# Kernel optimization log

Measured on AMD Instinct MI355X. Metric: run time of the kernel, lower is better.

## Reference

```python
import jax, jax.numpy as jnp
from jax import lax
import numpy as np

H = 20  # hardcoded n_hidden in the module


def _lstm_layer(xs, W_ih, W_hh, b):
    """xs: [T, B, F] -> hs: [T, B, H]. PyTorch gate order i,f,g,o."""
    B = xs.shape[1]
    h0 = jnp.zeros((B, H), xs.dtype)
    c0 = jnp.zeros((B, H), xs.dtype)

    def step(carry, x_t):
        h, c = carry
        g = x_t @ W_ih.T + h @ W_hh.T + b  # [B, 4H]
        i, f, gg, o = jnp.split(g, 4, axis=-1)
        c = jax.nn.sigmoid(f) * c + jax.nn.sigmoid(i) * jnp.tanh(gg)
        h = jax.nn.sigmoid(o) * jnp.tanh(c)
        return (h, c), h

    _, hs = lax.scan(step, (h0, c0), xs)
    return hs


def setup_inputs() -> dict:
    key = jax.random.key(0)
    ks = jax.random.split(key, 9)
    B, T, F, C = 1024, 512, 64, 10
    s_in = 1.0 / np.sqrt(H)
    return {
        "x": jax.random.normal(ks[0], (B, T, F), jnp.float32),
        "W_ih0": jax.random.uniform(ks[1], (4 * H, F), jnp.float32, -s_in, s_in),
        "W_hh0": jax.random.uniform(ks[2], (4 * H, H), jnp.float32, -s_in, s_in),
        "b0": jax.random.uniform(ks[3], (4 * H,), jnp.float32, -s_in, s_in),
        "W_ih1": jax.random.uniform(ks[4], (4 * H, H), jnp.float32, -s_in, s_in),
        "W_hh1": jax.random.uniform(ks[5], (4 * H, H), jnp.float32, -s_in, s_in),
        "b1": jax.random.uniform(ks[6], (4 * H,), jnp.float32, -s_in, s_in),
        "W_fc": jax.random.uniform(ks[7], (C, H * T), jnp.float32, -0.01, 0.01),
        "b_fc": jax.random.uniform(ks[8], (C,), jnp.float32, -0.01, 0.01),
    }


def reference(x, W_ih0, W_hh0, b0, W_ih1, W_hh1, b1, W_fc, b_fc):
    B = x.shape[0]
    xs = jnp.transpose(x, (1, 0, 2))          # [T, B, F]
    hs = _lstm_layer(xs, W_ih0, W_hh0, b0)    # [T, B, H]
    hs = _lstm_layer(hs, W_ih1, W_hh1, b1)    # [T, B, H]
    flat = jnp.transpose(hs, (1, 0, 2)).reshape(B, -1)  # [B, T*H]
    return flat @ W_fc.T + b_fc
```

## Files before the change

kernel.cpp:

```cpp
#include <hip/hip_runtime.h>

#define T_STEPS 512
#define F_IN    64
#define HID     20
#define NCLS    10
#define BATCH   1024

typedef __attribute__((ext_vector_type(8))) short bf16x8;
typedef __attribute__((ext_vector_type(4))) float f32x4;
typedef __attribute__((ext_vector_type(2))) float f32x2;

__device__ __forceinline__ float rcpf(float x) { return __builtin_amdgcn_rcpf(x); }
__device__ __forceinline__ float bperm(int idxBytes, float v) {
    return __int_as_float(__builtin_amdgcn_ds_bpermute(idxBytes, __float_as_int(v)));
}
__device__ __forceinline__ unsigned short bf16h(float v) {
    unsigned u = __float_as_uint(v);
    return (unsigned short)((u + 0x7fffu + ((u >> 16) & 1u)) >> 16);
}
__device__ __forceinline__ float bf16f(unsigned short h) {
    return __uint_as_float(((unsigned)h) << 16);
}
__device__ __forceinline__ f32x2 pkfma(f32x2 a, f32x2 b, f32x2 c) {
    f32x2 d;
    asm("v_pk_fma_f32 %0, %1, %2, %3" : "=v"(d) : "v"(a), "v"(b), "v"(c));
    return d;
}

extern "C" __global__ __launch_bounds__(256, 2)
void zgemm_mfma(const float* __restrict__ x, const float* __restrict__ W,
                const float* __restrict__ b0, float* __restrict__ Z)
{
    __shared__ unsigned short xlds[4][2][32][72];

    const int tid = threadIdx.x;
    const int w   = tid >> 6;
    const int l   = tid & 63;
    const int ar  = l & 15;
    const int aq  = l >> 4;
    const size_t R0 = ((size_t)blockIdx.x * 4 + w) * 32;

    const float* xw = x + R0 * F_IN;
    #pragma unroll
    for (int i = 0; i < 8; ++i) {
        const int idx = (i << 6) + l;
        const int row = idx >> 4;
        const int c4  = idx & 15;
        const float4 v = *(const float4*)(xw + (row << 6) + (c4 << 2));
        const unsigned short h0 = bf16h(v.x), h1 = bf16h(v.y),
                             h2 = bf16h(v.z), h3 = bf16h(v.w);
        const unsigned short g0 = bf16h(v.x - bf16f(h0)), g1 = bf16h(v.y - bf16f(h1)),
                             g2 = bf16h(v.z - bf16f(h2)), g3 = bf16h(v.w - bf16f(h3));
        *(uint2*)&xlds[w][0][row][c4 << 2] =
            make_uint2((unsigned)h0 | ((unsigned)h1 << 16), (unsigned)h2 | ((unsigned)h3 << 16));
        *(uint2*)&xlds[w][1][row][c4 << 2] =
            make_uint2((unsigned)g0 | ((unsigned)g1 << 16), (unsigned)g2 | ((unsigned)g3 << 16));
    }
    __syncthreads();

    bf16x8 af[2][2][2];
    #pragma unroll
    for (int m = 0; m < 2; ++m)
        #pragma unroll
        for (int s = 0; s < 2; ++s) {
            af[m][s][0] = *(const bf16x8*)&xlds[w][0][m * 16 + ar][aq * 8 + s * 32];
            af[m][s][1] = *(const bf16x8*)&xlds[w][1][m * 16 + ar][aq * 8 + s * 32];
        }

    bf16x8 bfr[5][2][2];
    #pragma unroll
    for (int n = 0; n < 5; ++n)
        #pragma unroll
        for (int s = 0; s < 2; ++s) {
            const float* wp = W + (size_t)(n * 16 + ar) * F_IN + aq * 8 + s * 32;
            const float4 u = *(const float4*)wp;
            const float4 v = *(const float4*)(wp + 4);
            bf16x8 hf, gf;
            hf[0] = (short)bf16h(u.x); gf[0] = (short)bf16h(u.x - bf16f(bf16h(u.x)));
            hf[1] = (short)bf16h(u.y); gf[1] = (short)bf16h(u.y - bf16f(bf16h(u.y)));
            hf[2] = (short)bf16h(u.z); gf[2] = (short)bf16h(u.z - bf16f(bf16h(u.z)));
            hf[3] = (short)bf16h(u.w); gf[3] = (short)bf16h(u.w - bf16f(bf16h(u.w)));
            hf[4] = (short)bf16h(v.x); gf[4] = (short)bf16h(v.x - bf16f(bf16h(v.x)));
            hf[5] = (short)bf16h(v.y); gf[5] = (short)bf16h(v.y - bf16f(bf16h(v.y)));
            hf[6] = (short)bf16h(v.z); gf[6] = (short)bf16h(v.z - bf16f(bf16h(v.z)));
            hf[7] = (short)bf16h(v.w); gf[7] = (short)bf16h(v.w - bf16f(bf16h(v.w)));
            bfr[n][s][0] = hf;
            bfr[n][s][1] = gf;
        }

    #pragma unroll
    for (int m = 0; m < 2; ++m)
        #pragma unroll
        for (int n = 0; n < 5; ++n) {
            const float bb = b0[n * 16 + ar];
            f32x4 acc = {bb, bb, bb, bb};
            #pragma unroll
            for (int s = 0; s < 2; ++s) {
                acc = __builtin_amdgcn_mfma_f32_16x16x32_bf16(af[m][s][0], bfr[n][s][0], acc, 0, 0, 0);
                acc = __builtin_amdgcn_mfma_f32_16x16x32_bf16(af[m][s][0], bfr[n][s][1], acc, 0, 0, 0);
                acc = __builtin_amdgcn_mfma_f32_16x16x32_bf16(af[m][s][1], bfr[n][s][0], acc, 0, 0, 0);
            }
            float* zp = Z + (R0 + m * 16 + aq * 4) * 80 + n * 16 + ar;
            zp[0]   = acc[0];
            zp[80]  = acc[1];
            zp[160] = acc[2];
            zp[240] = acc[3];
        }
}

extern "C" __global__ __launch_bounds__(128, 2)
void lstm_rec(const float* __restrict__ Z0,
              const float* __restrict__ W_hh0,
              const float* __restrict__ W_ih1, const float* __restrict__ W_hh1,
              const float* __restrict__ b1,
              const float* __restrict__ W_fc, const float* __restrict__ b_fc,
              float* __restrict__ out)
{
    __shared__ float4 ringH0v[4][6];
    __shared__ float4 ringH1v[8][6];
    float* ringH0 = (float*)ringH0v;
    float* ringH1 = (float*)ringH1v;

    const int tid = threadIdx.x;
    const int l   = tid & 63;
    const int wid = tid >> 6;
    const int b   = blockIdx.x;
    const int g2  = 64 + (l & 15);
    const bool isG = (l >= 40 && l < 60);

    const float mnegP = isG ? -2.885390082f : -1.442695041f;
    const float sclP  = isG ? 2.0f : 1.0f;
    const float biaP  = isG ? -1.0f : 0.0f;

    const int idxF  = ((l + 20) & 63) << 2;
    const int idxG  = ((l + 40) & 63) << 2;
    const int idxO  = ((l + 60) & 63) << 2;
    const int idxOB = ((l -  4) & 63) << 2;

    for (int i = tid; i < 96; i += 128)  ringH0[i] = 0.f;
    for (int i = tid; i < 192; i += 128) ringH1[i] = 0.f;

    f32x2 wh0p2[10], wh0s2[10];
    float c0 = 0.f;
    float zpc = 0.f, zsc = 0.f, zpn = 0.f, zsn = 0.f;
    unsigned zP = 0, zS = 0;
    const char* Zb = (const char*)Z0;
    #define ZLD(o) (*(const float*)(Zb + (o)))
    f32x2 facc2 = {0.f, 0.f};
    float4 wfc = make_float4(0.f, 0.f, 0.f, 0.f);
    unsigned wfOff = 0;
    int c4off = 0;
    const char* Wfb = (const char*)W_fc;

    f32x2 wi1p2[10], wi1s2[10], wh1p2[10], wh1s2[10];
    float b1p = 0.f, b1s = 0.f;
    float c1 = 0.f;

    if (wid == 0) {
        const f32x2* p;
        p = (const f32x2*)(W_hh0 + l  * HID);
        #pragma unroll
        for (int k = 0; k < 10; ++k) wh0p2[k] = p[k];
        p = (const f32x2*)(W_hh0 + g2 * HID);
        #pragma unroll
        for (int k = 0; k < 10; ++k) wh0s2[k] = p[k];

        zP = (unsigned)((b * (T_STEPS * 80) + l) * 4);
        zS = (unsigned)((b * (T_STEPS * 80) + 64 + (l & 15)) * 4);
        zpc = ZLD(zP);       zsc = ZLD(zS);
        zpn = ZLD(zP + 320); zsn = ZLD(zS + 320);
        zP += 640; zS += 640;

        const int cls = (l < 50) ? (l / 5) : 0;
        const int c4  = (l < 50) ? (l % 5) : 0;
        c4off = c4 * 16;
        wfOff = (unsigned)((cls * (T_STEPS * HID) + c4 * 4) * 4);
    } else {
        const f32x2* p;
        p = (const f32x2*)(W_ih1 + l  * HID);
        #pragma unroll
        for (int k = 0; k < 10; ++k) wi1p2[k] = p[k];
        p = (const f32x2*)(W_ih1 + g2 * HID);
        #pragma unroll
        for (int k = 0; k < 10; ++k) wi1s2[k] = p[k];
        p = (const f32x2*)(W_hh1 + l  * HID);
        #pragma unroll
        for (int k = 0; k < 10; ++k) wh1p2[k] = p[k];
        p = (const f32x2*)(W_hh1 + g2 * HID);
        #pragma unroll
        for (int k = 0; k < 10; ++k) wh1s2[k] = p[k];
        b1p = b1[l];
        b1s = b1[g2];
    }
    __syncthreads();

    #pragma unroll 8
    for (int t = 0; t < T_STEPS + 4; ++t) {
        if (wid == 0) {
            const int sigma = t - 4;
            float4 wfn = make_float4(0.f, 0.f, 0.f, 0.f);
            if (t >= 3 && t < T_STEPS + 3) {
                wfn = *(const float4*)(Wfb + wfOff);
                wfOff += HID * 4;
            }
            if (t < T_STEPS) {
                const float zp = zpc, zs = zsc;
                zpc = zpn; zsc = zsn;
                if (t + 2 < T_STEPS) {
                    zpn = ZLD(zP); zsn = ZLD(zS);
                    zP += 320; zS += 320;
                }
                f32x2 h2[10];
                {
                    const f32x4* hp = (const f32x4*)(ringH0 + ((t + 3) & 3) * 24);
                    #pragma unroll
                    for (int k = 0; k < 5; ++k) {
                        const f32x4 v = hp[k];
                        h2[2 * k]     = __builtin_shufflevector(v, v, 0, 1);
                        h2[2 * k + 1] = __builtin_shufflevector(v, v, 2, 3);
                    }
                }
                f32x2 aP = {zp, 0.f}, aP1 = {0.f, 0.f};
                f32x2 aS = {zs, 0.f}, aS1 = {0.f, 0.f};
                #pragma unroll
                for (int j = 0; j < 5; ++j) {
                    aP  = pkfma(h2[j],     wh0p2[j],     aP);
                    aP1 = pkfma(h2[5 + j], wh0p2[5 + j], aP1);
                    aS  = pkfma(h2[j],     wh0s2[j],     aS);
                    aS1 = pkfma(h2[5 + j], wh0s2[5 + j], aS1);
                }
                const float a_p = (aP.x + aP1.x) + (aP.y + aP1.y);
                const float a_s = (aS.x + aS1.x) + (aS.y + aS1.y);
                const float actP = fmaf(rcpf(1.f + exp2f(a_p * mnegP)), sclP, biaP);
                const float actS = rcpf(1.f + exp2f(a_s * -1.442695041f));
                const float fv = bperm(idxF, actP), gv = bperm(idxG, actP);
                const float oA = bperm(idxO, actP), oB = bperm(idxOB, actS);
                const float ov = (l < 4) ? oA : oB;
                c0 = fmaf(fv, c0, actP * gv);
                const float h0v = ov * fmaf(rcpf(1.f + exp2f(c0 * -2.885390082f)), 2.f, -1.f);
                if (l < HID) ringH0[(t & 3) * 24 + l] = h0v;
            }
            if (sigma >= 0) {
                const float4 h1q = *(const float4*)((const char*)ringH1 +
                                                    ((sigma & 7) * 96) + c4off);
                facc2 = pkfma((f32x2){h1q.x, h1q.y}, (f32x2){wfc.x, wfc.y}, facc2);
                facc2 = pkfma((f32x2){h1q.z, h1q.w}, (f32x2){wfc.z, wfc.w}, facc2);
            }
            wfc = wfn;
        } else {
            const int tau = t - 2;
            if (tau >= 0 && tau < T_STEPS) {
                f32x2 h02[10], h12[10];
                {
                    const f32x4* hp = (const f32x4*)(ringH0 + (tau & 3) * 24);
                    const f32x4* hq = (const f32x4*)(ringH1 + ((tau + 7) & 7) * 24);
                    #pragma unroll
                    for (int k = 0; k < 5; ++k) {
                        const f32x4 v = hp[k];
                        const f32x4 u = hq[k];
                        h02[2 * k]     = __builtin_shufflevector(v, v, 0, 1);
                        h02[2 * k + 1] = __builtin_shufflevector(v, v, 2, 3);
                        h12[2 * k]     = __builtin_shufflevector(u, u, 0, 1);
                        h12[2 * k + 1] = __builtin_shufflevector(u, u, 2, 3);
                    }
                }
                f32x2 bP = {b1p, 0.f}, bP1 = {0.f, 0.f};
                f32x2 bS = {b1s, 0.f}, bS1 = {0.f, 0.f};
                #pragma unroll
                for (int j = 0; j < 5; ++j) {
                    bP  = pkfma(h12[j],     wh1p2[j],     bP);
                    bP1 = pkfma(h12[5 + j], wh1p2[5 + j], bP1);
                    bS  = pkfma(h12[j],     wh1s2[j],     bS);
                    bS1 = pkfma(h12[5 + j], wh1s2[5 + j], bS1);
                }
                #pragma unroll
                for (int j = 0; j < 5; ++j) {
                    bP  = pkfma(h02[j],     wi1p2[j],     bP);
                    bP1 = pkfma(h02[5 + j], wi1p2[5 + j], bP1);
                    bS  = pkfma(h02[j],     wi1s2[j],     bS);
                    bS1 = pkfma(h02[5 + j], wi1s2[5 + j], bS1);
                }
                const float b_p = (bP.x + bP1.x) + (bP.y + bP1.y);
                const float b_s = (bS.x + bS1.x) + (bS.y + bS1.y);
                const float actQ = fmaf(rcpf(1.f + exp2f(b_p * mnegP)), sclP, biaP);
                const float actT = rcpf(1.f + exp2f(b_s * -1.442695041f));
                const float fv = bperm(idxF, actQ), gv = bperm(idxG, actQ);
                const float oA = bperm(idxO, actQ), oB = bperm(idxOB, actT);
                const float ov = (l < 4) ? oA : oB;
                c1 = fmaf(fv, c1, actQ * gv);
                const float h1v = ov * fmaf(rcpf(1.f + exp2f(c1 * -2.885390082f)), 2.f, -1.f);
                if (l < HID) ringH1[(tau & 7) * 24 + l] = h1v;
            }
        }
        if (t & 1) {
            asm volatile("s_waitcnt lgkmcnt(0)" ::: "memory");
            __builtin_amdgcn_s_barrier();
            asm volatile("" ::: "memory");
        }
    }

    if (wid == 0) {
        const float f = facc2.x + facc2.y;
        float r = f;
        r += __shfl(f, l + 1);
        r += __shfl(f, l + 2);
        r += __shfl(f, l + 3);
        r += __shfl(f, l + 4);
        if (l < 50 && (l % 5) == 0)
            out[(size_t)b * NCLS + (l / 5)] = r + b_fc[l / 5];
    }
}

extern "C" void kernel_launch(void* const* d_in, const int* in_sizes, int n_in,
                              void* d_out, int out_size, void* d_ws, size_t ws_size,
                              hipStream_t stream) {
    const float* x     = (const float*)d_in[0];
    const float* W_ih0 = (const float*)d_in[1];
    const float* W_hh0 = (const float*)d_in[2];
    const float* b0    = (const float*)d_in[3];
    const float* W_ih1 = (const float*)d_in[4];
    const float* W_hh1 = (const float*)d_in[5];
    const float* b1    = (const float*)d_in[6];
    const float* W_fc  = (const float*)d_in[7];
    const float* b_fc  = (const float*)d_in[8];
    float* out = (float*)d_out;

    float* Z0 = (float*)d_ws;

    zgemm_mfma<<<dim3(4096), dim3(256), 0, stream>>>(x, W_ih0, b0, Z0);
    lstm_rec<<<dim3(BATCH), dim3(128), 0, stream>>>(Z0, W_hh0, W_ih1, W_hh1,
                                                    b1, W_fc, b_fc, out);
}
```

Measured before the change: 318.6 us.

## Interleave LSTM gate rows per quad and gather gates with DPP instead of bpermute

Gate rows are remapped so that each quad of lanes holds the i,f,g,o pre-activations for one hidden unit, and the gates are gathered with DPP quad broadcasts instead of LDS bpermute. Hidden units 16-19 are handled by a second duplicated set of accumulators. The h0 ring buffer is doubled, the layer-1 and FC skews are lengthened, and the block barrier now fires every 4 steps instead of every 2. The aim is to take the LDS-latency permute ops off the recurrent critical path and to synchronise less often. The cost is extra activation math for the second set and deeper ring buffers.

New measurement: 341.5 us. 1.07x slower.

```diff
diff --git a/kernel.cpp b/kernel.cpp
--- a/kernel.cpp
+++ b/kernel.cpp
@@ -11,9 +11,6 @@
 typedef __attribute__((ext_vector_type(2))) float f32x2;
 
 __device__ __forceinline__ float rcpf(float x) { return __builtin_amdgcn_rcpf(x); }
-__device__ __forceinline__ float bperm(int idxBytes, float v) {
-    return __int_as_float(__builtin_amdgcn_ds_bpermute(idxBytes, __float_as_int(v)));
-}
 __device__ __forceinline__ unsigned short bf16h(float v) {
     unsigned u = __float_as_uint(v);
     return (unsigned short)((u + 0x7fffu + ((u >> 16) & 1u)) >> 16);
@@ -25,6 +22,10 @@
     f32x2 d;
     asm("v_pk_fma_f32 %0, %1, %2, %3" : "=v"(d) : "v"(a), "v"(b), "v"(c));
     return d;
+}
+template<int CTRL>
+__device__ __forceinline__ float qb(float v) {
+    return __int_as_float(__builtin_amdgcn_mov_dpp(__float_as_int(v), CTRL, 0xF, 0xF, true));
 }
 
 extern "C" __global__ __launch_bounds__(256, 2)
@@ -116,7 +117,7 @@
               const float* __restrict__ W_fc, const float* __restrict__ b_fc,
               float* __restrict__ out)
 {
-    __shared__ float4 ringH0v[4][6];
+    __shared__ float4 ringH0v[8][6];
     __shared__ float4 ringH1v[8][6];
     float* ringH0 = (float*)ringH0v;
     float* ringH1 = (float*)ringH1v;
@@ -125,23 +126,20 @@
     const int l   = tid & 63;
     const int wid = tid >> 6;
     const int b   = blockIdx.x;
-    const int g2  = 64 + (l & 15);
-    const bool isG = (l >= 40 && l < 60);
+    const int p   = l & 3;
+    const int q   = l >> 2;
+    const int rp  = p * HID + q;
+    const int rsc = p * HID + 16 + (q & 3);
+    const bool isG = (p == 2);
 
     const float mnegP = isG ? -2.885390082f : -1.442695041f;
     const float sclP  = isG ? 2.0f : 1.0f;
     const float biaP  = isG ? -1.0f : 0.0f;
 
-    const int idxF  = ((l + 20) & 63) << 2;
-    const int idxG  = ((l + 40) & 63) << 2;
-    const int idxO  = ((l + 60) & 63) << 2;
-    const int idxOB = ((l -  4) & 63) << 2;
-
-    for (int i = tid; i < 96; i += 128)  ringH0[i] = 0.f;
-    for (int i = tid; i < 192; i += 128) ringH1[i] = 0.f;
+    for (int i = tid; i < 192; i += 128) { ringH0[i] = 0.f; ringH1[i] = 0.f; }
 
     f32x2 wh0p2[10], wh0s2[10];
-    float c0 = 0.f;
+    float c0p = 0.f, c0s = 0.f;
     float zpc = 0.f, zsc = 0.f, zpn = 0.f, zsn = 0.f;
     unsigned zP = 0, zS = 0;
     const char* Zb = (const char*)Z0;
@@ -154,19 +152,19 @@
 
     f32x2 wi1p2[10], wi1s2[10], wh1p2[10], wh1s2[10];
     float b1p = 0.f, b1s = 0.f;
-    float c1 = 0.f;
+    float c1p = 0.f, c1s = 0.f;
 
     if (wid == 0) {
-        const f32x2* p;
-        p = (const f32x2*)(W_hh0 + l  * HID);
-        #pragma unroll
-        for (int k = 0; k < 10; ++k) wh0p2[k] = p[k];
-        p = (const f32x2*)(W_hh0 + g2 * HID);
-        #pragma unroll
-        for (int k = 0; k < 10; ++k) wh0s2[k] = p[k];
-
-        zP = (unsigned)((b * (T_STEPS * 80) + l) * 4);
-        zS = (unsigned)((b * (T_STEPS * 80) + 64 + (l & 15)) * 4);
+        const f32x2* wp;
+        wp = (const f32x2*)(W_hh0 + rp * HID);
+        #pragma unroll
+        for (int k = 0; k < 10; ++k) wh0p2[k] = wp[k];
+        wp = (const f32x2*)(W_hh0 + rsc * HID);
+        #pragma unroll
+        for (int k = 0; k < 10; ++k) wh0s2[k] = wp[k];
+
+        zP = (unsigned)((b * (T_STEPS * 80) + rp) * 4);
+        zS = (unsigned)((b * (T_STEPS * 80) + rsc) * 4);
         zpc = ZLD(zP);       zsc = ZLD(zS);
         zpn = ZLD(zP + 320); zsn = ZLD(zS + 320);
         zP += 640; zS += 640;
@@ -176,30 +174,30 @@
         c4off = c4 * 16;
         wfOff = (unsigned)((cls * (T_STEPS * HID) + c4 * 4) * 4);
     } else {
-        const f32x2* p;
-        p = (const f32x2*)(W_ih1 + l  * HID);
-        #pragma unroll
-        for (int k = 0; k < 10; ++k) wi1p2[k] = p[k];
-        p = (const f32x2*)(W_ih1 + g2 * HID);
-        #pragma unroll
-        for (int k = 0; k < 10; ++k) wi1s2[k] = p[k];
-        p = (const f32x2*)(W_hh1 + l  * HID);
-        #pragma unroll
-        for (int k = 0; k < 10; ++k) wh1p2[k] = p[k];
-        p = (const f32x2*)(W_hh1 + g2 * HID);
-        #pragma unroll
-        for (int k = 0; k < 10; ++k) wh1s2[k] = p[k];
-        b1p = b1[l];
-        b1s = b1[g2];
+        const f32x2* wp;
+        wp = (const f32x2*)(W_ih1 + rp * HID);
+        #pragma unroll
+        for (int k = 0; k < 10; ++k) wi1p2[k] = wp[k];
+        wp = (const f32x2*)(W_ih1 + rsc * HID);
+        #pragma unroll
+        for (int k = 0; k < 10; ++k) wi1s2[k] = wp[k];
+        wp = (const f32x2*)(W_hh1 + rp * HID);
+        #pragma unroll
+        for (int k = 0; k < 10; ++k) wh1p2[k] = wp[k];
+        wp = (const f32x2*)(W_hh1 + rsc * HID);
+        #pragma unroll
+        for (int k = 0; k < 10; ++k) wh1s2[k] = wp[k];
+        b1p = b1[rp];
+        b1s = b1[rsc];
     }
     __syncthreads();
 
     #pragma unroll 8
-    for (int t = 0; t < T_STEPS + 4; ++t) {
+    for (int t = 0; t < T_STEPS + 8; ++t) {
         if (wid == 0) {
-            const int sigma = t - 4;
+            const int sigma = t - 8;
             float4 wfn = make_float4(0.f, 0.f, 0.f, 0.f);
-            if (t >= 3 && t < T_STEPS + 3) {
+            if (t >= 7 && t < T_STEPS + 7) {
                 wfn = *(const float4*)(Wfb + wfOff);
                 wfOff += HID * 4;
             }
@@ -212,7 +210,7 @@
                 }
                 f32x2 h2[10];
                 {
-                    const f32x4* hp = (const f32x4*)(ringH0 + ((t + 3) & 3) * 24);
+                    const f32x4* hp = (const f32x4*)(ringH0 + ((t + 7) & 7) * 24);
                     #pragma unroll
                     for (int k = 0; k < 5; ++k) {
                         const f32x4 v = hp[k];
@@ -232,13 +230,19 @@
                 const float a_p = (aP.x + aP1.x) + (aP.y + aP1.y);
                 const float a_s = (aS.x + aS1.x) + (aS.y + aS1.y);
                 const float actP = fmaf(rcpf(1.f + exp2f(a_p * mnegP)), sclP, biaP);
-                const float actS = rcpf(1.f + exp2f(a_s * -1.442695041f));
-                const float fv = bperm(idxF, actP), gv = bperm(idxG, actP);
-                const float oA = bperm(idxO, actP), oB = bperm(idxOB, actS);
-                const float ov = (l < 4) ? oA : oB;
-                c0 = fmaf(fv, c0, actP * gv);
-                const float h0v = ov * fmaf(rcpf(1.f + exp2f(c0 * -2.885390082f)), 2.f, -1.f);
-                if (l < HID) ringH0[(t & 3) * 24 + l] = h0v;
+                const float actS = fmaf(rcpf(1.f + exp2f(a_s * mnegP)), sclP, biaP);
+                const float iP = qb<0x00>(actP), fP = qb<0x55>(actP),
+                            gP = qb<0xAA>(actP), oP = qb<0xFF>(actP);
+                c0p = fmaf(fP, c0p, iP * gP);
+                const float hP = oP * fmaf(rcpf(1.f + exp2f(c0p * -2.885390082f)), 2.f, -1.f);
+                const float iS = qb<0x00>(actS), fS = qb<0x55>(actS),
+                            gS = qb<0xAA>(actS), oS = qb<0xFF>(actS);
+                c0s = fmaf(fS, c0s, iS * gS);
+                const float hS = oS * fmaf(rcpf(1.f + exp2f(c0s * -2.885390082f)), 2.f, -1.f);
+                if (p == 0) {
+                    ringH0[(t & 7) * 24 + q] = hP;
+                    if (l < 16) ringH0[(t & 7) * 24 + 16 + q] = hS;
+                }
             }
             if (sigma >= 0) {
                 const float4 h1q = *(const float4*)((const char*)ringH1 +
@@ -248,11 +252,11 @@
             }
             wfc = wfn;
         } else {
-            const int tau = t - 2;
+            const int tau = t - 4;
             if (tau >= 0 && tau < T_STEPS) {
                 f32x2 h02[10], h12[10];
                 {
-                    const f32x4* hp = (const f32x4*)(ringH0 + (tau & 3) * 24);
+                    const f32x4* hp = (const f32x4*)(ringH0 + (tau & 7) * 24);
                     const f32x4* hq = (const f32x4*)(ringH1 + ((tau + 7) & 7) * 24);
                     #pragma unroll
                     for (int k = 0; k < 5; ++k) {
@@ -283,16 +287,22 @@
                 const float b_p = (bP.x + bP1.x) + (bP.y + bP1.y);
                 const float b_s = (bS.x + bS1.x) + (bS.y + bS1.y);
                 const float actQ = fmaf(rcpf(1.f + exp2f(b_p * mnegP)), sclP, biaP);
-                const float actT = rcpf(1.f + exp2f(b_s * -1.442695041f));
-                const float fv = bperm(idxF, actQ), gv = bperm(idxG, actQ);
-                const float oA = bperm(idxO, actQ), oB = bperm(idxOB, actT);
-                const float ov = (l < 4) ? oA : oB;
-                c1 = fmaf(fv, c1, actQ * gv);
-                const float h1v = ov * fmaf(rcpf(1.f + exp2f(c1 * -2.885390082f)), 2.f, -1.f);
-                if (l < HID) ringH1[(tau & 7) * 24 + l] = h1v;
-            }
-        }
-        if (t & 1) {
+                const float actT = fmaf(rcpf(1.f + exp2f(b_s * mnegP)), sclP, biaP);
+                const float iP = qb<0x00>(actQ), fP = qb<0x55>(actQ),
+                            gP = qb<0xAA>(actQ), oP = qb<0xFF>(actQ);
+                c1p = fmaf(fP, c1p, iP * gP);
+                const float hP = oP * fmaf(rcpf(1.f + exp2f(c1p * -2.885390082f)), 2.f, -1.f);
+                const float iS = qb<0x00>(actT), fS = qb<0x55>(actT),
+                            gS = qb<0xAA>(actT), oS = qb<0xFF>(actT);
+                c1s = fmaf(fS, c1s, iS * gS);
+                const float hS = oS * fmaf(rcpf(1.f + exp2f(c1s * -2.885390082f)), 2.f, -1.f);
+                if (p == 0) {
+                    ringH1[(tau & 7) * 24 + q] = hP;
+                    if (l < 16) ringH1[(tau & 7) * 24 + 16 + q] = hS;
+                }
+            }
+        }
+        if ((t & 3) == 3) {
             asm volatile("s_waitcnt lgkmcnt(0)" ::: "memory");
             __builtin_amdgcn_s_barrier();
             asm volatile("" ::: "memory");
```

## Process two batch rows per block in LSTM recurrence with deeper pipeline

Applied to the files above, without the earlier changes.

Each recurrence block now handles two batch elements, interleaving their independent dependency chains inside each wave to expose instruction-level parallelism. Ring buffers are duplicated per element and deepened to 8 slots. The layer-1 and FC lags are lengthened accordingly, and the grid is halved. This trades thread-level parallelism (fewer resident waves) and higher register pressure for better latency hiding per wave.

After: 496.6 us. +55.9%, slower.

```diff
diff --git a/kernel.cpp b/kernel.cpp
--- a/kernel.cpp
+++ b/kernel.cpp
@@ -108,7 +108,7 @@
         }
 }
 
-extern "C" __global__ __launch_bounds__(128, 2)
+extern "C" __global__ __launch_bounds__(128, 1)
 void lstm_rec(const float* __restrict__ Z0,
               const float* __restrict__ W_hh0,
               const float* __restrict__ W_ih1, const float* __restrict__ W_hh1,
@@ -116,15 +116,15 @@
               const float* __restrict__ W_fc, const float* __restrict__ b_fc,
               float* __restrict__ out)
 {
-    __shared__ float4 ringH0v[4][6];
-    __shared__ float4 ringH1v[8][6];
+    __shared__ float4 ringH0v[2][8][6];
+    __shared__ float4 ringH1v[2][8][6];
     float* ringH0 = (float*)ringH0v;
     float* ringH1 = (float*)ringH1v;
 
     const int tid = threadIdx.x;
     const int l   = tid & 63;
     const int wid = tid >> 6;
-    const int b   = blockIdx.x;
+    const int bb  = blockIdx.x * 2;
     const int g2  = 64 + (l & 15);
     const bool isG = (l >= 40 && l < 60);
 
@@ -137,16 +137,15 @@
     const int idxO  = ((l + 60) & 63) << 2;
     const int idxOB = ((l -  4) & 63) << 2;
 
-    for (int i = tid; i < 96; i += 128)  ringH0[i] = 0.f;
-    for (int i = tid; i < 192; i += 128) ringH1[i] = 0.f;
+    for (int i = tid; i < 384; i += 128) { ringH0[i] = 0.f; ringH1[i] = 0.f; }
 
     f32x2 wh0p2[10], wh0s2[10];
-    float c0 = 0.f;
-    float zpc = 0.f, zsc = 0.f, zpn = 0.f, zsn = 0.f;
-    unsigned zP = 0, zS = 0;
+    float c0[2] = {0.f, 0.f};
+    float zpc[2], zsc[2], zpn[2], zsn[2];
+    unsigned zP[2], zS[2];
     const char* Zb = (const char*)Z0;
     #define ZLD(o) (*(const float*)(Zb + (o)))
-    f32x2 facc2 = {0.f, 0.f};
+    f32x2 facc[2] = {{0.f, 0.f}, {0.f, 0.f}};
     float4 wfc = make_float4(0.f, 0.f, 0.f, 0.f);
     unsigned wfOff = 0;
     int c4off = 0;
@@ -154,142 +153,180 @@
 
     f32x2 wi1p2[10], wi1s2[10], wh1p2[10], wh1s2[10];
     float b1p = 0.f, b1s = 0.f;
-    float c1 = 0.f;
+    float c1[2] = {0.f, 0.f};
 
     if (wid == 0) {
-        const f32x2* p;
-        p = (const f32x2*)(W_hh0 + l  * HID);
-        #pragma unroll
-        for (int k = 0; k < 10; ++k) wh0p2[k] = p[k];
-        p = (const f32x2*)(W_hh0 + g2 * HID);
-        #pragma unroll
-        for (int k = 0; k < 10; ++k) wh0s2[k] = p[k];
-
-        zP = (unsigned)((b * (T_STEPS * 80) + l) * 4);
-        zS = (unsigned)((b * (T_STEPS * 80) + 64 + (l & 15)) * 4);
-        zpc = ZLD(zP);       zsc = ZLD(zS);
-        zpn = ZLD(zP + 320); zsn = ZLD(zS + 320);
-        zP += 640; zS += 640;
+        const f32x2* wp;
+        wp = (const f32x2*)(W_hh0 + l  * HID);
+        #pragma unroll
+        for (int k = 0; k < 10; ++k) wh0p2[k] = wp[k];
+        wp = (const f32x2*)(W_hh0 + g2 * HID);
+        #pragma unroll
+        for (int k = 0; k < 10; ++k) wh0s2[k] = wp[k];
+
+        #pragma unroll
+        for (int e = 0; e < 2; ++e) {
+            zP[e] = (unsigned)(((bb + e) * (T_STEPS * 80) + l) * 4);
+            zS[e] = (unsigned)(((bb + e) * (T_STEPS * 80) + 64 + (l & 15)) * 4);
+            zpc[e] = ZLD(zP[e]);       zsc[e] = ZLD(zS[e]);
+            zpn[e] = ZLD(zP[e] + 320); zsn[e] = ZLD(zS[e] + 320);
+            zP[e] += 640; zS[e] += 640;
+        }
 
         const int cls = (l < 50) ? (l / 5) : 0;
         const int c4  = (l < 50) ? (l % 5) : 0;
         c4off = c4 * 16;
         wfOff = (unsigned)((cls * (T_STEPS * HID) + c4 * 4) * 4);
     } else {
-        const f32x2* p;
-        p = (const f32x2*)(W_ih1 + l  * HID);
-        #pragma unroll
-        for (int k = 0; k < 10; ++k) wi1p2[k] = p[k];
-        p = (const f32x2*)(W_ih1 + g2 * HID);
-        #pragma unroll
-        for (int k = 0; k < 10; ++k) wi1s2[k] = p[k];
-        p = (const f32x2*)(W_hh1 + l  * HID);
-        #pragma unroll
-        for (int k = 0; k < 10; ++k) wh1p2[k] = p[k];
-        p = (const f32x2*)(W_hh1 + g2 * HID);
-        #pragma unroll
-        for (int k = 0; k < 10; ++k) wh1s2[k] = p[k];
+        const f32x2* wp;
+        wp = (const f32x2*)(W_ih1 + l  * HID);
+        #pragma unroll
+        for (int k = 0; k < 10; ++k) wi1p2[k] = wp[k];
+        wp = (const f32x2*)(W_ih1 + g2 * HID);
+        #pragma unroll
+        for (int k = 0; k < 10; ++k) wi1s2[k] = wp[k];
+        wp = (const f32x2*)(W_hh1 + l  * HID);
+        #pragma unroll
+        for (int k = 0; k < 10; ++k) wh1p2[k] = wp[k];
+        wp = (const f32x2*)(W_hh1 + g2 * HID);
+        #pragma unroll
+        for (int k = 0; k < 10; ++k) wh1s2[k] = wp[k];
         b1p = b1[l];
         b1s = b1[g2];
     }
     __syncthreads();
 
-    #pragma unroll 8
-    for (int t = 0; t < T_STEPS + 4; ++t) {
+    #pragma unroll 4
+    for (int t = 0; t < T_STEPS + 8; ++t) {
         if (wid == 0) {
-            const int sigma = t - 4;
+            const int sigma = t - 8;
             float4 wfn = make_float4(0.f, 0.f, 0.f, 0.f);
-            if (t >= 3 && t < T_STEPS + 3) {
+            if (t >= 7 && t < T_STEPS + 7) {
                 wfn = *(const float4*)(Wfb + wfOff);
                 wfOff += HID * 4;
             }
             if (t < T_STEPS) {
-                const float zp = zpc, zs = zsc;
-                zpc = zpn; zsc = zsn;
+                float zp[2], zs[2];
+                #pragma unroll
+                for (int e = 0; e < 2; ++e) {
+                    zp[e] = zpc[e]; zs[e] = zsc[e];
+                    zpc[e] = zpn[e]; zsc[e] = zsn[e];
+                }
                 if (t + 2 < T_STEPS) {
-                    zpn = ZLD(zP); zsn = ZLD(zS);
-                    zP += 320; zS += 320;
-                }
-                f32x2 h2[10];
-                {
-                    const f32x4* hp = (const f32x4*)(ringH0 + ((t + 3) & 3) * 24);
+                    #pragma unroll
+                    for (int e = 0; e < 2; ++e) {
+                        zpn[e] = ZLD(zP[e]); zsn[e] = ZLD(zS[e]);
+                        zP[e] += 320; zS[e] += 320;
+                    }
+                }
+                f32x2 h2[2][10];
+                #pragma unroll
+                for (int e = 0; e < 2; ++e) {
+                    const f32x4* hp = (const f32x4*)(ringH0 + e * 192 + ((t + 7) & 7) * 24);
                     #pragma unroll
                     for (int k = 0; k < 5; ++k) {
                         const f32x4 v = hp[k];
-                        h2[2 * k]     = __builtin_shufflevector(v, v, 0, 1);
-                        h2[2 * k + 1] = __builtin_shufflevector(v, v, 2, 3);
-                    }
-                }
-                f32x2 aP = {zp, 0.f}, aP1 = {0.f, 0.f};
-                f32x2 aS = {zs, 0.f}, aS1 = {0.f, 0.f};
+                        h2[e][2 * k]     = __builtin_shufflevector(v, v, 0, 1);
+                        h2[e][2 * k + 1] = __builtin_shufflevector(v, v, 2, 3);
+                    }
+                }
+                f32x2 aP[2], aP1[2], aS[2], aS1[2];
+                #pragma unroll
+                for (int e = 0; e < 2; ++e) {
+                    aP[e] = (f32x2){zp[e], 0.f}; aP1[e] = (f32x2){0.f, 0.f};
+                    aS[e] = (f32x2){zs[e], 0.f}; aS1[e] = (f32x2){0.f, 0.f};
+                }
                 #pragma unroll
                 for (int j = 0; j < 5; ++j) {
-                    aP  = pkfma(h2[j],     wh0p2[j],     aP);
-                    aP1 = pkfma(h2[5 + j], wh0p2[5 + j], aP1);
-                    aS  = pkfma(h2[j],     wh0s2[j],     aS);
-                    aS1 = pkfma(h2[5 + j], wh0s2[5 + j], aS1);
-                }
-                const float a_p = (aP.x + aP1.x) + (aP.y + aP1.y);
-                const float a_s = (aS.x + aS1.x) + (aS.y + aS1.y);
-                const float actP = fmaf(rcpf(1.f + exp2f(a_p * mnegP)), sclP, biaP);
-                const float actS = rcpf(1.f + exp2f(a_s * -1.442695041f));
-                const float fv = bperm(idxF, actP), gv = bperm(idxG, actP);
-                const float oA = bperm(idxO, actP), oB = bperm(idxOB, actS);
-                const float ov = (l < 4) ? oA : oB;
-                c0 = fmaf(fv, c0, actP * gv);
-                const float h0v = ov * fmaf(rcpf(1.f + exp2f(c0 * -2.885390082f)), 2.f, -1.f);
-                if (l < HID) ringH0[(t & 3) * 24 + l] = h0v;
+                    #pragma unroll
+                    for (int e = 0; e < 2; ++e) {
+                        aP[e]  = pkfma(h2[e][j],     wh0p2[j],     aP[e]);
+                        aP1[e] = pkfma(h2[e][5 + j], wh0p2[5 + j], aP1[e]);
+                        aS[e]  = pkfma(h2[e][j],     wh0s2[j],     aS[e]);
+                        aS1[e] = pkfma(h2[e][5 + j], wh0s2[5 + j], aS1[e]);
+                    }
+                }
+                #pragma unroll
+                for (int e = 0; e < 2; ++e) {
+                    const float a_p = (aP[e].x + aP1[e].x) + (aP[e].y + aP1[e].y);
+                    const float a_s = (aS[e].x + aS1[e].x) + (aS[e].y + aS1[e].y);
+                    const float actP = fmaf(rcpf(1.f + exp2f(a_p * mnegP)), sclP, biaP);
+                    const float actS = rcpf(1.f + exp2f(a_s * -1.442695041f));
+                    const float fv = bperm(idxF, actP), gv = bperm(idxG, actP);
+                    const float oA = bperm(idxO, actP), oB = bperm(idxOB, actS);
+                    const float ov = (l < 4) ? oA : oB;
+                    c0[e] = fmaf(fv, c0[e], actP * gv);
+                    const float h0v = ov * fmaf(rcpf(1.f + exp2f(c0[e] * -2.885390082f)), 2.f, -1.f);
+                    if (l < HID) ringH0[e * 192 + (t & 7) * 24 + l] = h0v;
+                }
             }
             if (sigma >= 0) {
-                const float4 h1q = *(const float4*)((const char*)ringH1 +
-                                                    ((sigma & 7) * 96) + c4off);
-                facc2 = pkfma((f32x2){h1q.x, h1q.y}, (f32x2){wfc.x, wfc.y}, facc2);
-                facc2 = pkfma((f32x2){h1q.z, h1q.w}, (f32x2){wfc.z, wfc.w}, facc2);
+                #pragma unroll
+                for (int e = 0; e < 2; ++e) {
+                    const float4 h1q = *(const float4*)((const char*)ringH1 +
+                                                        e * 768 + ((sigma & 7) * 96) + c4off);
+                    facc[e] = pkfma((f32x2){h1q.x, h1q.y}, (f32x2){wfc.x, wfc.y}, facc[e]);
+                    facc[e] = pkfma((f32x2){h1q.z, h1q.w}, (f32x2){wfc.z, wfc.w}, facc[e]);
+                }
             }
             wfc = wfn;
         } else {
-            const int tau = t - 2;
+            const int tau = t - 4;
             if (tau >= 0 && tau < T_STEPS) {
-                f32x2 h02[10], h12[10];
-                {
-                    const f32x4* hp = (const f32x4*)(ringH0 + (tau & 3) * 24);
-                    const f32x4* hq = (const f32x4*)(ringH1 + ((tau + 7) & 7) * 24);
+                f32x2 h02[2][10], h12[2][10];
+                #pragma unroll
+                for (int e = 0; e < 2; ++e) {
+                    const f32x4* hp = (const f32x4*)(ringH0 + e * 192 + (tau & 7) * 24);
+                    const f32x4* hq = (const f32x4*)(ringH1 + e * 192 + ((tau + 7) & 7) * 24);
                     #pragma unroll
                     for (int k = 0; k < 5; ++k) {
                         const f32x4 v = hp[k];
                         const f32x4 u = hq[k];
-                        h02[2 * k]     = __builtin_shufflevector(v, v, 0, 1);
-                        h02[2 * k + 1] = __builtin_shufflevector(v, v, 2, 3);
-                        h12[2 * k]     = __builtin_shufflevector(u, u, 0, 1);
-                        h12[2 * k + 1] = __builtin_shufflevector(u, u, 2, 3);
-                    }
-                }
-                f32x2 bP = {b1p, 0.f}, bP1 = {0.f, 0.f};
-                f32x2 bS = {b1s, 0.f}, bS1 = {0.f, 0.f};
+                        h02[e][2 * k]     = __builtin_shufflevector(v, v, 0, 1);
+                        h02[e][2 * k + 1] = __builtin_shufflevector(v, v, 2, 3);
+                        h12[e][2 * k]     = __builtin_shufflevector(u, u, 0, 1);
+                        h12[e][2 * k + 1] = __builtin_shufflevector(u, u, 2, 3);
+                    }
+                }
+                f32x2 bP[2], bP1[2], bS[2], bS1[2];
+                #pragma unroll
+                for (int e = 0; e < 2; ++e) {
+                    bP[e] = (f32x2){b1p, 0.f}; bP1[e] = (f32x2){0.f, 0.f};
+                    bS[e] = (f32x2){b1s, 0.f}; bS1[e] = (f32x2){0.f, 0.f};
+                }
                 #pragma unroll
                 for (int j = 0; j < 5; ++j) {
-                    bP  = pkfma(h12[j],     wh1p2[j],     bP);
-                    bP1 = pkfma(h12[5 + j], wh1p2[5 + j], bP1);
-                    bS  = pkfma(h12[j],     wh1s2[j],     bS);
-                    bS1 = pkfma(h12[5 + j], wh1s2[5 + j], bS1);
+                    #pragma unroll
+                    for (int e = 0; e < 2; ++e) {
+                        bP[e]  = pkfma(h12[e][j],     wh1p2[j],     bP[e]);
+                        bP1[e] = pkfma(h12[e][5 + j], wh1p2[5 + j], bP1[e]);
+                        bS[e]  = pkfma(h12[e][j],     wh1s2[j],     bS[e]);
+                        bS1[e] = pkfma(h12[e][5 + j], wh1s2[5 + j], bS1[e]);
+                    }
                 }
                 #pragma unroll
                 for (int j = 0; j < 5; ++j) {
-                    bP  = pkfma(h02[j],     wi1p2[j],     bP);
-                    bP1 = pkfma(h02[5 + j], wi1p2[5 + j], bP1);
-                    bS  = pkfma(h02[j],     wi1s2[j],     bS);
-                    bS1 = pkfma(h02[5 + j], wi1s2[5 + j], bS1);
-                }
-                const float b_p = (bP.x + bP1.x) + (bP.y + bP1.y);
-                const float b_s = (bS.x + bS1.x) + (bS.y + bS1.y);
-                const float actQ = fmaf(rcpf(1.f + exp2f(b_p * mnegP)), sclP, biaP);
-                const float actT = rcpf(1.f + exp2f(b_s * -1.442695041f));
-                const float fv = bperm(idxF, actQ), gv = bperm(idxG, actQ);
-                const float oA = bperm(idxO, actQ), oB = bperm(idxOB, actT);
-                const float ov = (l < 4) ? oA : oB;
-                c1 = fmaf(fv, c1, actQ * gv);
-                const float h1v = ov * fmaf(rcpf(1.f + exp2f(c1 * -2.885390082f)), 2.f, -1.f);
-                if (l < HID) ringH1[(tau & 7) * 24 + l] = h1v;
+                    #pragma unroll
+                    for (int e = 0; e < 2; ++e) {
+                        bP[e]  = pkfma(h02[e][j],     wi1p2[j],     bP[e]);
+                        bP1[e] = pkfma(h02[e][5 + j], wi1p2[5 + j], bP1[e]);
+                        bS[e]  = pkfma(h02[e][j],     wi1s2[j],     bS[e]);
+                        bS1[e] = pkfma(h02[e][5 + j], wi1s2[5 + j], bS1[e]);
+                    }
+                }
+                #pragma unroll
+                for (int e = 0; e < 2; ++e) {
+                    const float b_p = (bP[e].x + bP1[e].x) + (bP[e].y + bP1[e].y);
+                    const float b_s = (bS[e].x + bS1[e].x) + (bS[e].y + bS1[e].y);
+                    const float actQ = fmaf(rcpf(1.f + exp2f(b_p * mnegP)), sclP, biaP);
+                    const float actT = rcpf(1.f + exp2f(b_s * -1.442695041f));
+                    const float fv = bperm(idxF, actQ), gv = bperm(idxG, actQ);
+                    const float oA = bperm(idxO, actQ), oB = bperm(idxOB, actT);
+                    const float ov = (l < 4) ? oA : oB;
+                    c1[e] = fmaf(fv, c1[e], actQ * gv);
+                    const float h1v = ov * fmaf(rcpf(1.f + exp2f(c1[e] * -2.885390082f)), 2.f, -1.f);
+                    if (l < HID) ringH1[e * 192 + (tau & 7) * 24 + l] = h1v;
+                }
             }
         }
         if (t & 1) {
@@ -300,14 +337,17 @@
     }
 
     if (wid == 0) {
-        const float f = facc2.x + facc2.y;
-        float r = f;
-        r += __shfl(f, l + 1);
-        r += __shfl(f, l + 2);
-        r += __shfl(f, l + 3);
-        r += __shfl(f, l + 4);
-        if (l < 50 && (l % 5) == 0)
-            out[(size_t)b * NCLS + (l / 5)] = r + b_fc[l / 5];
+        #pragma unroll
+        for (int e = 0; e < 2; ++e) {
+            const float f = facc[e].x + facc[e].y;
+            float r = f;
+            r += __shfl(f, l + 1);
+            r += __shfl(f, l + 2);
+            r += __shfl(f, l + 3);
+            r += __shfl(f, l + 4);
+            if (l < 50 && (l % 5) == 0)
+                out[(size_t)(bb + e) * NCLS + (l / 5)] = r + b_fc[l / 5];
+        }
     }
 }
 
@@ -328,6 +368,6 @@
     float* Z0 = (float*)d_ws;
 
     zgemm_mfma<<<dim3(4096), dim3(256), 0, stream>>>(x, W_ih0, b0, Z0);
-    lstm_rec<<<dim3(BATCH), dim3(128), 0, stream>>>(Z0, W_hh0, W_ih1, W_hh1,
-                                                    b1, W_fc, b_fc, out);
-}
+    lstm_rec<<<dim3(BATCH / 2), dim3(128), 0, stream>>>(Z0, W_hh0, W_ih1, W_hh1,
+                                                        b1, W_fc, b_fc, out);
+}
```

## Fuse input projection GEMM into recurrent kernel with producer wave and LDS ring

Applied to the files above, without the earlier changes.

Removes the separate zgemm kernel and its Z0 workspace round-trip through global memory. A third wave per block now computes the layer-0 input projection in 16-timestep chunks with MFMA and writes them into a 3-chunk LDS ring, which the layer-0 wave reads in place of global loads. The GEMM work overlaps the latency-bound recurrence, at the cost of more threads and LDS per block, lower occupancy bounds (192 threads, 3 blocks), and a producer wave that adds work to the barrier-paced loop.

Result: slower. 1.026 ms (+222.0%).

```diff
diff --git a/kernel.cpp b/kernel.cpp
--- a/kernel.cpp
+++ b/kernel.cpp
@@ -26,96 +26,26 @@
     asm("v_pk_fma_f32 %0, %1, %2, %3" : "=v"(d) : "v"(a), "v"(b), "v"(c));
     return d;
 }
-
-extern "C" __global__ __launch_bounds__(256, 2)
-void zgemm_mfma(const float* __restrict__ x, const float* __restrict__ W,
-                const float* __restrict__ b0, float* __restrict__ Z)
-{
-    __shared__ unsigned short xlds[4][2][32][72];
-
-    const int tid = threadIdx.x;
-    const int w   = tid >> 6;
-    const int l   = tid & 63;
-    const int ar  = l & 15;
-    const int aq  = l >> 4;
-    const size_t R0 = ((size_t)blockIdx.x * 4 + w) * 32;
-
-    const float* xw = x + R0 * F_IN;
+__device__ __forceinline__ void mk8(const float4 u, const float4 v, bf16x8& h, bf16x8& g) {
+    const float vv[8] = {u.x, u.y, u.z, u.w, v.x, v.y, v.z, v.w};
     #pragma unroll
     for (int i = 0; i < 8; ++i) {
-        const int idx = (i << 6) + l;
-        const int row = idx >> 4;
-        const int c4  = idx & 15;
-        const float4 v = *(const float4*)(xw + (row << 6) + (c4 << 2));
-        const unsigned short h0 = bf16h(v.x), h1 = bf16h(v.y),
-                             h2 = bf16h(v.z), h3 = bf16h(v.w);
-        const unsigned short g0 = bf16h(v.x - bf16f(h0)), g1 = bf16h(v.y - bf16f(h1)),
-                             g2 = bf16h(v.z - bf16f(h2)), g3 = bf16h(v.w - bf16f(h3));
-        *(uint2*)&xlds[w][0][row][c4 << 2] =
-            make_uint2((unsigned)h0 | ((unsigned)h1 << 16), (unsigned)h2 | ((unsigned)h3 << 16));
-        *(uint2*)&xlds[w][1][row][c4 << 2] =
-            make_uint2((unsigned)g0 | ((unsigned)g1 << 16), (unsigned)g2 | ((unsigned)g3 << 16));
-    }
-    __syncthreads();
-
-    bf16x8 af[2][2][2];
-    #pragma unroll
-    for (int m = 0; m < 2; ++m)
-        #pragma unroll
-        for (int s = 0; s < 2; ++s) {
-            af[m][s][0] = *(const bf16x8*)&xlds[w][0][m * 16 + ar][aq * 8 + s * 32];
-            af[m][s][1] = *(const bf16x8*)&xlds[w][1][m * 16 + ar][aq * 8 + s * 32];
-        }
-
-    bf16x8 bfr[5][2][2];
-    #pragma unroll
-    for (int n = 0; n < 5; ++n)
-        #pragma unroll
-        for (int s = 0; s < 2; ++s) {
-            const float* wp = W + (size_t)(n * 16 + ar) * F_IN + aq * 8 + s * 32;
-            const float4 u = *(const float4*)wp;
-            const float4 v = *(const float4*)(wp + 4);
-            bf16x8 hf, gf;
-            hf[0] = (short)bf16h(u.x); gf[0] = (short)bf16h(u.x - bf16f(bf16h(u.x)));
-            hf[1] = (short)bf16h(u.y); gf[1] = (short)bf16h(u.y - bf16f(bf16h(u.y)));
-            hf[2] = (short)bf16h(u.z); gf[2] = (short)bf16h(u.z - bf16f(bf16h(u.z)));
-            hf[3] = (short)bf16h(u.w); gf[3] = (short)bf16h(u.w - bf16f(bf16h(u.w)));
-            hf[4] = (short)bf16h(v.x); gf[4] = (short)bf16h(v.x - bf16f(bf16h(v.x)));
-            hf[5] = (short)bf16h(v.y); gf[5] = (short)bf16h(v.y - bf16f(bf16h(v.y)));
-            hf[6] = (short)bf16h(v.z); gf[6] = (short)bf16h(v.z - bf16f(bf16h(v.z)));
-            hf[7] = (short)bf16h(v.w); gf[7] = (short)bf16h(v.w - bf16f(bf16h(v.w)));
-            bfr[n][s][0] = hf;
-            bfr[n][s][1] = gf;
-        }
-
-    #pragma unroll
-    for (int m = 0; m < 2; ++m)
-        #pragma unroll
-        for (int n = 0; n < 5; ++n) {
-            const float bb = b0[n * 16 + ar];
-            f32x4 acc = {bb, bb, bb, bb};
-            #pragma unroll
-            for (int s = 0; s < 2; ++s) {
-                acc = __builtin_amdgcn_mfma_f32_16x16x32_bf16(af[m][s][0], bfr[n][s][0], acc, 0, 0, 0);
-                acc = __builtin_amdgcn_mfma_f32_16x16x32_bf16(af[m][s][0], bfr[n][s][1], acc, 0, 0, 0);
-                acc = __builtin_amdgcn_mfma_f32_16x16x32_bf16(af[m][s][1], bfr[n][s][0], acc, 0, 0, 0);
-            }
-            float* zp = Z + (R0 + m * 16 + aq * 4) * 80 + n * 16 + ar;
-            zp[0]   = acc[0];
-            zp[80]  = acc[1];
-            zp[160] = acc[2];
-            zp[240] = acc[3];
-        }
-}
-
-extern "C" __global__ __launch_bounds__(128, 2)
-void lstm_rec(const float* __restrict__ Z0,
-              const float* __restrict__ W_hh0,
-              const float* __restrict__ W_ih1, const float* __restrict__ W_hh1,
-              const float* __restrict__ b1,
-              const float* __restrict__ W_fc, const float* __restrict__ b_fc,
-              float* __restrict__ out)
+        const unsigned short hh = bf16h(vv[i]);
+        h[i] = (short)hh;
+        g[i] = (short)bf16h(vv[i] - bf16f(hh));
+    }
+}
+
+extern "C" __global__ __launch_bounds__(192, 3)
+void lstm_fused(const float* __restrict__ x,
+                const float* __restrict__ W_ih0, const float* __restrict__ W_hh0,
+                const float* __restrict__ b0,
+                const float* __restrict__ W_ih1, const float* __restrict__ W_hh1,
+                const float* __restrict__ b1,
+                const float* __restrict__ W_fc, const float* __restrict__ b_fc,
+                float* __restrict__ out)
 {
+    __shared__ float zring[48 * 80];
     __shared__ float4 ringH0v[4][6];
     __shared__ float4 ringH1v[8][6];
     float* ringH0 = (float*)ringH0v;
@@ -137,15 +67,12 @@
     const int idxO  = ((l + 60) & 63) << 2;
     const int idxOB = ((l -  4) & 63) << 2;
 
-    for (int i = tid; i < 96; i += 128)  ringH0[i] = 0.f;
-    for (int i = tid; i < 192; i += 128) ringH1[i] = 0.f;
+    for (int i = tid; i < 96; i += 192)  ringH0[i] = 0.f;
+    for (int i = tid; i < 192; i += 192) ringH1[i] = 0.f;
 
     f32x2 wh0p2[10], wh0s2[10];
     float c0 = 0.f;
-    float zpc = 0.f, zsc = 0.f, zpn = 0.f, zsn = 0.f;
-    unsigned zP = 0, zS = 0;
-    const char* Zb = (const char*)Z0;
-    #define ZLD(o) (*(const float*)(Zb + (o)))
+    float zpc = 0.f, zsc = 0.f;
     f32x2 facc2 = {0.f, 0.f};
     float4 wfc = make_float4(0.f, 0.f, 0.f, 0.f);
     unsigned wfOff = 0;
@@ -156,43 +83,91 @@
     float b1p = 0.f, b1s = 0.f;
     float c1 = 0.f;
 
+    bf16x8 bfr[5][2][2];
+    float  bb5[5];
+    float4 xu0, xv0, xu1, xv1;
+    const int ar = l & 15, aq = l >> 4;
+    const float* xb = x + (size_t)b * T_STEPS * F_IN;
+
+    auto loadx = [&](int c) {
+        const float* xp = xb + (c * 16 + ar) * F_IN + aq * 8;
+        xu0 = *(const float4*)(xp);
+        xv0 = *(const float4*)(xp + 4);
+        xu1 = *(const float4*)(xp + 32);
+        xv1 = *(const float4*)(xp + 36);
+    };
+    auto zchunk = [&](int c) {
+        bf16x8 ah[2], al[2];
+        mk8(xu0, xv0, ah[0], al[0]);
+        mk8(xu1, xv1, ah[1], al[1]);
+        const int rbase = (c % 3) * 16;
+        #pragma unroll
+        for (int n = 0; n < 5; ++n) {
+            f32x4 acc = {bb5[n], bb5[n], bb5[n], bb5[n]};
+            #pragma unroll
+            for (int s = 0; s < 2; ++s) {
+                acc = __builtin_amdgcn_mfma_f32_16x16x32_bf16(ah[s], bfr[n][s][0], acc, 0, 0, 0);
+                acc = __builtin_amdgcn_mfma_f32_16x16x32_bf16(ah[s], bfr[n][s][1], acc, 0, 0, 0);
+                acc = __builtin_amdgcn_mfma_f32_16x16x32_bf16(al[s], bfr[n][s][0], acc, 0, 0, 0);
+            }
+            float* zp = zring + (rbase + aq * 4) * 80 + n * 16 + ar;
+            zp[0]   = acc[0];
+            zp[80]  = acc[1];
+            zp[160] = acc[2];
+            zp[240] = acc[3];
+        }
+    };
+
     if (wid == 0) {
-        const f32x2* p;
-        p = (const f32x2*)(W_hh0 + l  * HID);
-        #pragma unroll
-        for (int k = 0; k < 10; ++k) wh0p2[k] = p[k];
-        p = (const f32x2*)(W_hh0 + g2 * HID);
-        #pragma unroll
-        for (int k = 0; k < 10; ++k) wh0s2[k] = p[k];
-
-        zP = (unsigned)((b * (T_STEPS * 80) + l) * 4);
-        zS = (unsigned)((b * (T_STEPS * 80) + 64 + (l & 15)) * 4);
-        zpc = ZLD(zP);       zsc = ZLD(zS);
-        zpn = ZLD(zP + 320); zsn = ZLD(zS + 320);
-        zP += 640; zS += 640;
+        const f32x2* wp;
+        wp = (const f32x2*)(W_hh0 + l  * HID);
+        #pragma unroll
+        for (int k = 0; k < 10; ++k) wh0p2[k] = wp[k];
+        wp = (const f32x2*)(W_hh0 + g2 * HID);
+        #pragma unroll
+        for (int k = 0; k < 10; ++k) wh0s2[k] = wp[k];
 
         const int cls = (l < 50) ? (l / 5) : 0;
         const int c4  = (l < 50) ? (l % 5) : 0;
         c4off = c4 * 16;
         wfOff = (unsigned)((cls * (T_STEPS * HID) + c4 * 4) * 4);
-    } else {
-        const f32x2* p;
-        p = (const f32x2*)(W_ih1 + l  * HID);
-        #pragma unroll
-        for (int k = 0; k < 10; ++k) wi1p2[k] = p[k];
-        p = (const f32x2*)(W_ih1 + g2 * HID);
-        #pragma unroll
-        for (int k = 0; k < 10; ++k) wi1s2[k] = p[k];
-        p = (const f32x2*)(W_hh1 + l  * HID);
-        #pragma unroll
-        for (int k = 0; k < 10; ++k) wh1p2[k] = p[k];
-        p = (const f32x2*)(W_hh1 + g2 * HID);
-        #pragma unroll
-        for (int k = 0; k < 10; ++k) wh1s2[k] = p[k];
+    } else if (wid == 1) {
+        const f32x2* wp;
+        wp = (const f32x2*)(W_ih1 + l  * HID);
+        #pragma unroll
+        for (int k = 0; k < 10; ++k) wi1p2[k] = wp[k];
+        wp = (const f32x2*)(W_ih1 + g2 * HID);
+        #pragma unroll
+        for (int k = 0; k < 10; ++k) wi1s2[k] = wp[k];
+        wp = (const f32x2*)(W_hh1 + l  * HID);
+        #pragma unroll
+        for (int k = 0; k < 10; ++k) wh1p2[k] = wp[k];
+        wp = (const f32x2*)(W_hh1 + g2 * HID);
+        #pragma unroll
+        for (int k = 0; k < 10; ++k) wh1s2[k] = wp[k];
         b1p = b1[l];
         b1s = b1[g2];
+    } else {
+        #pragma unroll
+        for (int n = 0; n < 5; ++n) {
+            #pragma unroll
+            for (int s = 0; s < 2; ++s) {
+                const float* wp = W_ih0 + (size_t)(n * 16 + ar) * F_IN + aq * 8 + s * 32;
+                mk8(*(const float4*)wp, *(const float4*)(wp + 4),
+                    bfr[n][s][0], bfr[n][s][1]);
+            }
+            bb5[n] = b0[n * 16 + ar];
+        }
+        loadx(0); zchunk(0);
+        loadx(1); zchunk(1);
+        loadx(2);
     }
     __syncthreads();
+
+    if (wid == 0) {
+        zpc = zring[l];
+        zsc = zring[64 + (l & 15)];
+    }
 
     #pragma unroll 8
     for (int t = 0; t < T_STEPS + 4; ++t) {
@@ -205,10 +180,11 @@
             }
             if (t < T_STEPS) {
                 const float zp = zpc, zs = zsc;
-                zpc = zpn; zsc = zsn;
-                if (t + 2 < T_STEPS) {
-                    zpn = ZLD(zP); zsn = ZLD(zS);
-                    zP += 320; zS += 320;
+                if (t + 1 < T_STEPS) {
+                    const unsigned tn = (unsigned)(t + 1);
+                    const unsigned rb = ((tn >> 4) % 3u) * 16 + (tn & 15u);
+                    zpc = zring[rb * 80 + l];
+                    zsc = zring[rb * 80 + 64 + (l & 15)];
                 }
                 f32x2 h2[10];
                 {
@@ -247,7 +223,7 @@
                 facc2 = pkfma((f32x2){h1q.z, h1q.w}, (f32x2){wfc.z, wfc.w}, facc2);
             }
             wfc = wfn;
-        } else {
+        } else if (wid == 1) {
             const int tau = t - 2;
             if (tau >= 0 && tau < T_STEPS) {
                 f32x2 h02[10], h12[10];
@@ -291,6 +267,14 @@
                 const float h1v = ov * fmaf(rcpf(1.f + exp2f(c1 * -2.885390082f)), 2.f, -1.f);
                 if (l < HID) ringH1[(tau & 7) * 24 + l] = h1v;
             }
+        } else {
+            if ((t & 15) == 0) {
+                const int c = (t >> 4) + 2;
+                if (c < 32) {
+                    zchunk(c);
+                    if (c + 1 < 32) loadx(c + 1);
+                }
+            }
         }
         if (t & 1) {
             asm volatile("s_waitcnt lgkmcnt(0)" ::: "memory");
@@ -325,9 +309,6 @@
     const float* b_fc  = (const float*)d_in[8];
     float* out = (float*)d_out;
 
-    float* Z0 = (float*)d_ws;
-
-    zgemm_mfma<<<dim3(4096), dim3(256), 0, stream>>>(x, W_ih0, b0, Z0);
-    lstm_rec<<<dim3(BATCH), dim3(128), 0, stream>>>(Z0, W_hh0, W_ih1, W_hh1,
-                                                    b1, W_fc, b_fc, out);
-}
+    lstm_fused<<<dim3(BATCH), dim3(192), 0, stream>>>(
+        x, W_ih0, W_hh0, b0, W_ih1, W_hh1, b1, W_fc, b_fc, out);
+}
```
